# Kernel tuning notes

Hardware: AMD Instinct MI355X
Metric: run time of the kernel (lower is better)

The kernel has to match this reference:

```python
import jax, jax.numpy as jnp
import numpy as np
from jax import lax

B, T, QD, ED, AD = 256, 512, 1024, 512, 128
NF, KS = 32, 31  # location filters, kernel size
PAD = (KS - 1) // 2


def setup_inputs() -> dict:
    key = jax.random.key(0)
    ks = jax.random.split(key, 12)
    query = jax.random.normal(ks[0], (B, QD), jnp.float32)
    inputs = jax.random.normal(ks[1], (B, T, ED), jnp.float32)
    processed_inputs = jax.random.normal(ks[2], (B, T, AD), jnp.float32)
    mask = jnp.ones((B, T), jnp.bool_)
    # init_states()
    attention_weights = jnp.zeros((B, T), jnp.float32)
    attention_weights_cum = jnp.zeros((B, T), jnp.float32)
    alpha = jnp.concatenate([jnp.ones((B, 1)), jnp.full((B, T - 1), 1e-7)], axis=1).astype(jnp.float32)
    u = 0.5 * jnp.ones((B, 1), jnp.float32)
    # parameters (xavier-ish scale)
    Wq = jax.random.normal(ks[3], (QD, AD), jnp.float32) * 0.03
    conv_w = jax.random.normal(ks[4], (NF, 2, KS), jnp.float32) * 0.1  # OIH
    Wloc = jax.random.normal(ks[5], (NF, AD), jnp.float32) * 0.1
    v_w = jax.random.normal(ks[6], (AD, 1), jnp.float32) * 0.1
    v_b = jnp.zeros((1,), jnp.float32)
    ta_w = jax.random.normal(ks[7], (ED + QD, 1), jnp.float32) * 0.02
    ta_b = jnp.zeros((1,), jnp.float32)
    return dict(query=query, inputs=inputs, processed_inputs=processed_inputs, mask=mask,
                attention_weights=attention_weights, attention_weights_cum=attention_weights_cum,
                alpha=alpha, u=u, Wq=Wq, conv_w=conv_w, Wloc=Wloc, v_w=v_w, v_b=v_b,
                ta_w=ta_w, ta_b=ta_b)


def reference(query, inputs, processed_inputs, mask, attention_weights,
              attention_weights_cum, alpha, u, Wq, conv_w, Wloc, v_w, v_b, ta_w, ta_b):
    # location-sensitive energies
    att_cat = jnp.stack([attention_weights, attention_weights_cum], axis=1)  # [B,2,T]
    loc = lax.conv_general_dilated(att_cat, conv_w, (1,), [(PAD, PAD)],
                                   dimension_numbers=('NCH', 'OIH', 'NCH'))  # [B,NF,T]
    proc_attn = jnp.einsum('bft,fa->bta', loc, Wloc)                         # [B,T,AD]
    proc_query = (query @ Wq)[:, None, :]                                    # [B,1,AD]
    energies = (jnp.tanh(proc_query + proc_attn + processed_inputs) @ v_w + v_b)[..., 0]  # [B,T]
    energies = jnp.where(mask, energies, -jnp.inf)
    alignment = jax.nn.softmax(energies, axis=-1)
    # forward attention recursion (training mode, no forward_attn_mask)
    shifted = jnp.pad(alpha[:, :-1], ((0, 0), (1, 0)))
    alpha_new = ((1.0 - u) * alpha + u * shifted + 1e-8) * alignment
    alpha_new = alpha_new / jnp.sum(alpha_new, axis=1, keepdims=True)
    context = jnp.einsum('bt,btd->bd', alpha_new, inputs)                    # [B,ED]
    # transition agent (state update; computed for faithfulness)
    u_new = jax.nn.sigmoid(jnp.concatenate([context, query], axis=-1) @ ta_w + ta_b)
    del u_new
    return context
```

## Files before the change

### kernel.cpp

```cpp
#include <hip/hip_runtime.h>

#define BB 256
#define TT 512
#define QD 1024
#define ED 512
#define AD 128
#define NF 32
#define KS 31
#define PADL 15
#define TCHUNK 256

typedef float f32x4 __attribute__((ext_vector_type(4)));

__device__ __forceinline__ float tanh_fast(float x) {
    float ex = __expf(2.0f * x);
    return 1.0f - 2.0f / (ex + 1.0f);
}

__device__ __forceinline__ float dpp_xor1(float x) {
    int y = __builtin_amdgcn_update_dpp(0, __float_as_int(x), 0xB1, 0xF, 0xF, true);
    return x + __int_as_float(y);
}
__device__ __forceinline__ float dpp_xor2(float x) {
    int y = __builtin_amdgcn_update_dpp(0, __float_as_int(x), 0x4E, 0xF, 0xF, true);
    return x + __int_as_float(y);
}
__device__ __forceinline__ float dpp_xor4(float x) {
    int y = __builtin_amdgcn_update_dpp(0, __float_as_int(x), 0x141, 0xF, 0xF, true);
    return x + __int_as_float(y);
}
__device__ __forceinline__ float dpp_xor8(float x) {
    int y = __builtin_amdgcn_update_dpp(0, __float_as_int(x), 0x140, 0xF, 0xF, true);
    return x + __int_as_float(y);
}
__device__ __forceinline__ float wave_sum64(float x) {
    x = dpp_xor1(x);
    x = dpp_xor2(x);
    x = dpp_xor4(x);
    x = dpp_xor8(x);
    int xi = __float_as_int(x);
    float r0  = __int_as_float(__builtin_amdgcn_readlane(xi, 0));
    float r16 = __int_as_float(__builtin_amdgcn_readlane(xi, 16));
    float r32 = __int_as_float(__builtin_amdgcn_readlane(xi, 32));
    float r48 = __int_as_float(__builtin_amdgcn_readlane(xi, 48));
    return (r0 + r16) + (r32 + r48);
}

__global__ __launch_bounds__(256) void k_pq(const float* __restrict__ query,
                                            const float* __restrict__ Wq,
                                            float* __restrict__ pq) {
    int b = blockIdx.x;
    int tid = threadIdx.x;
    __shared__ float qs[QD];
    __shared__ float part[256];
    for (int i = tid; i < QD; i += 256) qs[i] = query[(size_t)b * QD + i];
    __syncthreads();
    int half = tid >> 7;
    int a = tid & 127;
    int kbase = half * 512;
    const float* wp = Wq + (size_t)kbase * AD + a;
    float acc = 0.f;
#pragma unroll 8
    for (int k = 0; k < 512; ++k)
        acc = fmaf(qs[kbase + k], wp[(size_t)k * AD], acc);
    part[tid] = acc;
    __syncthreads();
    if (tid < 128) pq[(size_t)b * AD + tid] = part[tid] + part[tid + 128];
}

__global__ __launch_bounds__(256) void k_energies(
    const float* __restrict__ attW, const float* __restrict__ attC,
    const float* __restrict__ convw, const float* __restrict__ Wloc,
    const float* __restrict__ pq, const float* __restrict__ pin,
    const float* __restrict__ vw, const float* __restrict__ vb,
    const float* __restrict__ alpha, const float* __restrict__ uArr,
    float* __restrict__ qOut) {
    int b = blockIdx.x;
    int t0 = blockIdx.y * TCHUNK;
    int tid = threadIdx.x;

    __shared__ float sA[TCHUNK + 2 * PADL];
    __shared__ float sC[TCHUNK + 2 * PADL];
    __shared__ float sAl[TCHUNK + 1];
    __shared__ float sLoc[TCHUNK * 36];

    for (int i = tid; i < TCHUNK + 2 * PADL; i += 256) {
        int t = t0 + i - PADL;
        float a = 0.f, c = 0.f;
        if (t >= 0 && t < TT) {
            a = attW[(size_t)b * TT + t];
            c = attC[(size_t)b * TT + t];
        }
        sA[i] = a;
        sC[i] = c;
    }
    for (int i = tid; i < TCHUNK + 1; i += 256) {
        int t = t0 + i - 1;
        sAl[i] = (t >= 0) ? alpha[(size_t)b * TT + t] : 0.f;
    }
    __syncthreads();

    {
        float winA[KS], winC[KS];
#pragma unroll
        for (int k = 0; k < KS; ++k) {
            winA[k] = sA[tid + k];
            winC[k] = sC[tid + k];
        }
        float* lrow = sLoc + tid * 36;
        for (int f = 0; f < NF; ++f) {
            const float* cwa = convw + f * (2 * KS);
            float acc = 0.f;
#pragma unroll
            for (int k = 0; k < KS; ++k) {
                acc = fmaf(cwa[k], winA[k], acc);
                acc = fmaf(cwa[KS + k], winC[k], acc);
            }
            lrow[f] = acc;
        }
    }
    __syncthreads();

    int wid = tid >> 6, lane = tid & 63;
    float2 w2[NF];
#pragma unroll
    for (int f = 0; f < NF; ++f)
        w2[f] = ((const float2*)(Wloc + f * AD))[lane];
    float2 pq2 = ((const float2*)(pq + (size_t)b * AD))[lane];
    float2 vw2 = ((const float2*)vw)[lane];
    float vbv = vb[0];
    float u = uArr[b];

    for (int tt = wid; tt < TCHUNK; tt += 4) {
        int t = t0 + tt;
        const float4* lr = (const float4*)(sLoc + tt * 36);
        float pa0 = 0.f, pa1 = 0.f;
#pragma unroll
        for (int j = 0; j < 8; ++j) {
            float4 Lv = lr[j];
            pa0 = fmaf(Lv.x, w2[4 * j + 0].x, pa0);
            pa1 = fmaf(Lv.x, w2[4 * j + 0].y, pa1);
            pa0 = fmaf(Lv.y, w2[4 * j + 1].x, pa0);
            pa1 = fmaf(Lv.y, w2[4 * j + 1].y, pa1);
            pa0 = fmaf(Lv.z, w2[4 * j + 2].x, pa0);
            pa1 = fmaf(Lv.z, w2[4 * j + 2].y, pa1);
            pa0 = fmaf(Lv.w, w2[4 * j + 3].x, pa0);
            pa1 = fmaf(Lv.w, w2[4 * j + 3].y, pa1);
        }
        float2 p2 = ((const float2*)pin)[(size_t)(b * TT + t) * (AD / 2) + lane];
        float x0 = pq2.x + pa0 + p2.x;
        float x1 = pq2.y + pa1 + p2.y;
        float epart = tanh_fast(x0) * vw2.x + tanh_fast(x1) * vw2.y;
        float e = wave_sum64(epart);
        if (lane == 0) {
            float w = fmaf(1.f - u, sAl[tt + 1], u * sAl[tt] + 1e-8f);
            qOut[(size_t)b * TT + t] = w * __expf(e + vbv);
        }
    }
}

__global__ __launch_bounds__(1024) void k_ctx(
    const float* __restrict__ qIn, const float* __restrict__ inputs,
    float* __restrict__ out) {
    int b = blockIdx.x;
    int tid = threadIdx.x;
    int lane = tid & 63, wid = tid >> 6;

    __shared__ float al[TT];
    __shared__ float red[16];
    __shared__ f32x4 sacc[8][128];

    size_t base = (size_t)b * TT;
    float q = 0.f;
    if (tid < TT) {
        q = qIn[base + tid];
        al[tid] = q;
    }
    float s = wave_sum64(q);
    if (lane == 0) red[wid] = s;
    __syncthreads();
    s = 0.f;
#pragma unroll
    for (int i = 0; i < 16; ++i) s += red[i];

    int g = tid >> 7;
    int c = tid & 127;
    const f32x4* in4 = (const f32x4*)inputs;
    size_t rb = ((size_t)b * TT + (size_t)g * 64) * (ED / 4) + c;
    f32x4 acc = (f32x4)(0.f);
#pragma unroll 16
    for (int j = 0; j < 64; ++j) {
        f32x4 v = __builtin_nontemporal_load(&in4[rb + (size_t)j * (ED / 4)]);
        float w = al[g * 64 + j];
        acc.x = fmaf(w, v.x, acc.x);
        acc.y = fmaf(w, v.y, acc.y);
        acc.z = fmaf(w, v.z, acc.z);
        acc.w = fmaf(w, v.w, acc.w);
    }
    sacc[g][c] = acc;
    __syncthreads();
    if (tid < 128) {
        f32x4 t = sacc[0][tid];
#pragma unroll
        for (int i = 1; i < 8; ++i) t += sacc[i][tid];
        float inv = 1.f / s;
        t.x *= inv; t.y *= inv; t.z *= inv; t.w *= inv;
        ((f32x4*)out)[(size_t)b * (ED / 4) + tid] = t;
    }
}

extern "C" void kernel_launch(void* const* d_in, const int* in_sizes, int n_in,
                              void* d_out, int out_size, void* d_ws, size_t ws_size,
                              hipStream_t stream) {
    (void)in_sizes; (void)n_in; (void)out_size; (void)ws_size;
    const float* query = (const float*)d_in[0];
    const float* inputs = (const float*)d_in[1];
    const float* pin   = (const float*)d_in[2];
    const float* attW  = (const float*)d_in[4];
    const float* attC  = (const float*)d_in[5];
    const float* alpha = (const float*)d_in[6];
    const float* uArr  = (const float*)d_in[7];
    const float* Wq    = (const float*)d_in[8];
    const float* convw = (const float*)d_in[9];
    const float* Wloc  = (const float*)d_in[10];
    const float* vw    = (const float*)d_in[11];
    const float* vb    = (const float*)d_in[12];

    float* ws = (float*)d_ws;
    float* pq   = ws;
    float* qBuf = pq + BB * AD;

    k_pq<<<dim3(BB), dim3(256), 0, stream>>>(query, Wq, pq);
    k_energies<<<dim3(BB, TT / TCHUNK), dim3(256), 0, stream>>>(
        attW, attC, convw, Wloc, pq, pin, vw, vb, alpha, uArr, qBuf);
    k_ctx<<<dim3(BB), dim3(1024), 0, stream>>>(qBuf, inputs, (float*)d_out);
}
```

Before: 120.4 us.

## Compute energies one timestep per thread with a pre-transposed Wloc

The energies kernel now assigns one timestep to each thread instead of one timestep per wavefront. Each thread keeps its 32 location-conv outputs in registers and loops over all 128 attention dims itself, using a Wloc transposed by an extra block of the pq kernel. This removes the shared-memory loc staging, a barrier and the per-timestep wave reductions, and the Wloc, pq and v reads become wave-uniform. The cost is that each thread streams its own 512-byte processed_inputs row, so a wavefront's loads hit many scattered rows instead of being coalesced, and register pressure rises.

```diff
diff --git a/kernel.cpp b/kernel.cpp
--- a/kernel.cpp
+++ b/kernel.cpp
@@ -34,10 +34,7 @@
     return x + __int_as_float(y);
 }
 __device__ __forceinline__ float wave_sum64(float x) {
-    x = dpp_xor1(x);
-    x = dpp_xor2(x);
-    x = dpp_xor4(x);
-    x = dpp_xor8(x);
+    x = dpp_xor1(x); x = dpp_xor2(x); x = dpp_xor4(x); x = dpp_xor8(x);
     int xi = __float_as_int(x);
     float r0  = __int_as_float(__builtin_amdgcn_readlane(xi, 0));
     float r16 = __int_as_float(__builtin_amdgcn_readlane(xi, 16));
@@ -46,11 +43,19 @@
     return (r0 + r16) + (r32 + r48);
 }
 
-__global__ __launch_bounds__(256) void k_pq(const float* __restrict__ query,
-                                            const float* __restrict__ Wq,
-                                            float* __restrict__ pq) {
+__global__ __launch_bounds__(256) void k_pq_prep(
+    const float* __restrict__ query, const float* __restrict__ Wq,
+    const float* __restrict__ Wloc, float* __restrict__ pq,
+    float* __restrict__ WlocT) {
     int b = blockIdx.x;
     int tid = threadIdx.x;
+    if (b == BB) {
+        for (int idx = tid; idx < NF * AD; idx += 256) {
+            int a = idx >> 5, f = idx & 31;
+            WlocT[idx] = Wloc[f * AD + a];
+        }
+        return;
+    }
     __shared__ float qs[QD];
     __shared__ float part[256];
     for (int i = tid; i < QD; i += 256) qs[i] = query[(size_t)b * QD + i];
@@ -68,9 +73,9 @@
     if (tid < 128) pq[(size_t)b * AD + tid] = part[tid] + part[tid + 128];
 }
 
-__global__ __launch_bounds__(256) void k_energies(
+__global__ __launch_bounds__(256) void k_en(
     const float* __restrict__ attW, const float* __restrict__ attC,
-    const float* __restrict__ convw, const float* __restrict__ Wloc,
+    const float* __restrict__ convw, const float* __restrict__ WlocT,
     const float* __restrict__ pq, const float* __restrict__ pin,
     const float* __restrict__ vw, const float* __restrict__ vb,
     const float* __restrict__ alpha, const float* __restrict__ uArr,
@@ -78,28 +83,24 @@
     int b = blockIdx.x;
     int t0 = blockIdx.y * TCHUNK;
     int tid = threadIdx.x;
+    int t = t0 + tid;
 
     __shared__ float sA[TCHUNK + 2 * PADL];
     __shared__ float sC[TCHUNK + 2 * PADL];
-    __shared__ float sAl[TCHUNK + 1];
-    __shared__ float sLoc[TCHUNK * 36];
 
     for (int i = tid; i < TCHUNK + 2 * PADL; i += 256) {
-        int t = t0 + i - PADL;
+        int tg = t0 + i - PADL;
         float a = 0.f, c = 0.f;
-        if (t >= 0 && t < TT) {
-            a = attW[(size_t)b * TT + t];
-            c = attC[(size_t)b * TT + t];
+        if (tg >= 0 && tg < TT) {
+            a = attW[(size_t)b * TT + tg];
+            c = attC[(size_t)b * TT + tg];
         }
         sA[i] = a;
         sC[i] = c;
     }
-    for (int i = tid; i < TCHUNK + 1; i += 256) {
-        int t = t0 + i - 1;
-        sAl[i] = (t >= 0) ? alpha[(size_t)b * TT + t] : 0.f;
-    }
-    __syncthreads();
-
+    __syncthreads();
+
+    float loc[NF];
     {
         float winA[KS], winC[KS];
 #pragma unroll
@@ -107,7 +108,6 @@
             winA[k] = sA[tid + k];
             winC[k] = sC[tid + k];
         }
-        float* lrow = sLoc + tid * 36;
         for (int f = 0; f < NF; ++f) {
             const float* cwa = convw + f * (2 * KS);
             float acc = 0.f;
@@ -116,47 +116,41 @@
                 acc = fmaf(cwa[k], winA[k], acc);
                 acc = fmaf(cwa[KS + k], winC[k], acc);
             }
-            lrow[f] = acc;
-        }
-    }
-    __syncthreads();
-
-    int wid = tid >> 6, lane = tid & 63;
-    float2 w2[NF];
-#pragma unroll
-    for (int f = 0; f < NF; ++f)
-        w2[f] = ((const float2*)(Wloc + f * AD))[lane];
-    float2 pq2 = ((const float2*)(pq + (size_t)b * AD))[lane];
-    float2 vw2 = ((const float2*)vw)[lane];
-    float vbv = vb[0];
+            loc[f] = acc;
+        }
+    }
+
+    const float* pqRow = pq + (size_t)b * AD;
+    const float* pinRow = pin + ((size_t)b * TT + t) * AD;
+    float e = 0.f;
+    for (int a4 = 0; a4 < AD / 4; ++a4) {
+        float4 p4 = *(const float4*)(pinRow + a4 * 4);
+        float pe[4];
+#pragma unroll
+        for (int j = 0; j < 4; ++j) {
+            int a = a4 * 4 + j;
+            const float* wc = WlocT + a * NF;
+            float pa = 0.f;
+#pragma unroll
+            for (int f = 0; f < NF; ++f)
+                pa = fmaf(loc[f], wc[f], pa);
+            pe[j] = pa;
+        }
+        float x0 = pqRow[a4 * 4 + 0] + pe[0] + p4.x;
+        float x1 = pqRow[a4 * 4 + 1] + pe[1] + p4.y;
+        float x2 = pqRow[a4 * 4 + 2] + pe[2] + p4.z;
+        float x3 = pqRow[a4 * 4 + 3] + pe[3] + p4.w;
+        e = fmaf(tanh_fast(x0), vw[a4 * 4 + 0], e);
+        e = fmaf(tanh_fast(x1), vw[a4 * 4 + 1], e);
+        e = fmaf(tanh_fast(x2), vw[a4 * 4 + 2], e);
+        e = fmaf(tanh_fast(x3), vw[a4 * 4 + 3], e);
+    }
+
     float u = uArr[b];
-
-    for (int tt = wid; tt < TCHUNK; tt += 4) {
-        int t = t0 + tt;
-        const float4* lr = (const float4*)(sLoc + tt * 36);
-        float pa0 = 0.f, pa1 = 0.f;
-#pragma unroll
-        for (int j = 0; j < 8; ++j) {
-            float4 Lv = lr[j];
-            pa0 = fmaf(Lv.x, w2[4 * j + 0].x, pa0);
-            pa1 = fmaf(Lv.x, w2[4 * j + 0].y, pa1);
-            pa0 = fmaf(Lv.y, w2[4 * j + 1].x, pa0);
-            pa1 = fmaf(Lv.y, w2[4 * j + 1].y, pa1);
-            pa0 = fmaf(Lv.z, w2[4 * j + 2].x, pa0);
-            pa1 = fmaf(Lv.z, w2[4 * j + 2].y, pa1);
-            pa0 = fmaf(Lv.w, w2[4 * j + 3].x, pa0);
-            pa1 = fmaf(Lv.w, w2[4 * j + 3].y, pa1);
-        }
-        float2 p2 = ((const float2*)pin)[(size_t)(b * TT + t) * (AD / 2) + lane];
-        float x0 = pq2.x + pa0 + p2.x;
-        float x1 = pq2.y + pa1 + p2.y;
-        float epart = tanh_fast(x0) * vw2.x + tanh_fast(x1) * vw2.y;
-        float e = wave_sum64(epart);
-        if (lane == 0) {
-            float w = fmaf(1.f - u, sAl[tt + 1], u * sAl[tt] + 1e-8f);
-            qOut[(size_t)b * TT + t] = w * __expf(e + vbv);
-        }
-    }
+    float aC = alpha[(size_t)b * TT + t];
+    float aP = (t > 0) ? alpha[(size_t)b * TT + t - 1] : 0.f;
+    float wq = fmaf(1.f - u, aC, u * aP + 1e-8f);
+    qOut[(size_t)b * TT + t] = wq * __expf(e + vb[0]);
 }
 
 __global__ __launch_bounds__(1024) void k_ctx(
@@ -227,11 +221,12 @@
     const float* vb    = (const float*)d_in[12];
 
     float* ws = (float*)d_ws;
-    float* pq   = ws;
-    float* qBuf = pq + BB * AD;
-
-    k_pq<<<dim3(BB), dim3(256), 0, stream>>>(query, Wq, pq);
-    k_energies<<<dim3(BB, TT / TCHUNK), dim3(256), 0, stream>>>(
-        attW, attC, convw, Wloc, pq, pin, vw, vb, alpha, uArr, qBuf);
+    float* pq    = ws;
+    float* WlocT = pq + BB * AD;
+    float* qBuf  = WlocT + NF * AD;
+
+    k_pq_prep<<<dim3(BB + 1), dim3(256), 0, stream>>>(query, Wq, Wloc, pq, WlocT);
+    k_en<<<dim3(BB, TT / TCHUNK), dim3(256), 0, stream>>>(
+        attW, attC, convw, WlocT, pq, pin, vw, vb, alpha, uArr, qBuf);
     k_ctx<<<dim3(BB), dim3(1024), 0, stream>>>(qBuf, inputs, (float*)d_out);
 }
```

Result: slower. 123.4 us (+2.5%).
